# Kernel tuning notes

Hardware: AMD Instinct MI355X
Metric: run time of the kernel (lower is better)

The kernel has to match this reference:

```python
import jax, jax.numpy as jnp
import numpy as np

N, D, C, S = 100000, 512, 4096, 50000


def setup_inputs() -> dict:
    key = jax.random.key(0)
    k1, k2 = jax.random.split(key)
    X = jax.random.normal(k1, (N, D), dtype=jnp.float32)
    codebook_sum = jax.random.normal(k2, (C, D), dtype=jnp.float32)
    prompt_mask = jnp.arange(N) < S  # first S rows are support (True), rest are queries
    return {"X": X, "codebook_sum": codebook_sum, "prompt_mask": prompt_mask, "num_support": S}


def reference(X, codebook_sum, prompt_mask, num_support):
    # num_support is a static Python int (replaces torch.nonzero(prompt_mask) dynamic split)
    s = num_support
    support = X[:s]                                   # [S, D] support (prompt_mask==True)
    query = X[s:]                                     # [Q, D] queries (prompt_mask==False)
    # dense similarity matmul + top-1 nearest-codebook search + gather
    cos_sim = jnp.einsum('sd,cd->sc', support, codebook_sum)  # [S, C]
    top_idx = jnp.argmax(cos_sim, axis=1)             # [S]
    code_n = codebook_sum[top_idx]                    # [S, D] gathered nearest codes
    # mean-pooled prototypes broadcast over queries
    proto = jnp.mean(support, axis=0)                 # [D]
    proto_code = jnp.mean(code_n, axis=0)             # [D]
    # euclidean distances to each prototype
    query_score = jnp.sqrt(jnp.sum((query - proto) ** 2, axis=1))        # [Q]
    query_score_code = jnp.sqrt(jnp.sum((query - proto_code) ** 2, axis=1))  # [Q]
    return (query_score + query_score_code) / 2
```

## Files before the change

### kernel.cpp

```cpp
#include <hip/hip_runtime.h>
#include <hip/hip_bf16.h>

#define NTOT 100000
#define DIM  512
#define CB   4096
#define SSUP 50000
#define NQ   (NTOT - SSUP)

#define MTILES 391
#define MPAD   (MTILES * 128)
#define NTILES 32

typedef __bf16 bf16x8 __attribute__((ext_vector_type(8)));
typedef __bf16 bf16x4 __attribute__((ext_vector_type(4)));
typedef float  f32x4  __attribute__((ext_vector_type(4)));

#define OFF_CBBF   0
#define OFF_XB     4194304
#define OFF_PV     55443456
#define OFF_PI     61849600
#define OFF_PSUM   68255744
#define OFF_PCSUM  68257792
#define OFF_HIST   68259840
#define OFF_TIDX   68276224
#define WS_NEED    (68276224 + 200000)
#define ZERO_BYTES (2048 + 2048 + 16384)

#define F_OFF_PSUM   4194304
#define F_OFF_PCSUM  4196352
#define F_OFF_HIST   4198400
#define F_OFF_TIDX   4214784

__device__ __forceinline__ void load_lds16(const void* g, void* l) {
    __builtin_amdgcn_global_load_lds(
        (const __attribute__((address_space(1))) void*)g,
        (__attribute__((address_space(3))) void*)l, 16, 0, 0);
}

__global__ void k_convert(const float* __restrict__ src, __bf16* __restrict__ dst) {
    int i = (blockIdx.x * 256 + threadIdx.x) * 4;
    float4 v = *(const float4*)(src + i);
    bf16x4 o;
    o[0] = (__bf16)v.x; o[1] = (__bf16)v.y; o[2] = (__bf16)v.z; o[3] = (__bf16)v.w;
    *(bf16x4*)(dst + i) = o;
}

__global__ void k_proto_sum(const float* __restrict__ X, float* __restrict__ protoSum) {
    const int d = threadIdx.x;
    const int r0 = blockIdx.x * 500;
    float acc = 0.f;
    for (int r = r0; r < r0 + 500; ++r)
        acc += X[(size_t)r * DIM + d];
    atomicAdd(&protoSum[d], acc);
}

__global__ __launch_bounds__(256)
void k_gemm_tile(const __bf16* __restrict__ Xb, const __bf16* __restrict__ cbb,
                 float* __restrict__ pv, int* __restrict__ pi)
{
    __shared__ __bf16 lA[128 * 32];
    __shared__ __bf16 lB[128 * 32];
    __shared__ float  sv[128][2];
    __shared__ int    si[128][2];

    const int tid  = threadIdx.x;
    const int wave = tid >> 6;
    const int lane = tid & 63;
    const int wm   = wave >> 1;
    const int wn   = wave & 1;
    const int l15  = lane & 15;
    const int q    = lane >> 4;
    const int nt   = blockIdx.x;
    const int mt   = blockIdx.y;
    const size_t r0 = (size_t)mt * 128;
    const int    c0 = nt * 128;

    f32x4 acc[4][4];
    #pragma unroll
    for (int i = 0; i < 4; ++i)
        #pragma unroll
        for (int j = 0; j < 4; ++j)
            acc[i][j] = (f32x4){0.f, 0.f, 0.f, 0.f};

    for (int k0 = 0; k0 < 512; k0 += 32) {
        __syncthreads();
        #pragma unroll
        for (int i = 0; i < 2; ++i) {
            const int ck  = i * 256 + tid;
            const int row = ck >> 2;
            const int kc  = ck & 3;
            load_lds16(Xb  + (r0 + row) * DIM + k0 + kc * 8, lA + ck * 8);
            load_lds16(cbb + (size_t)(c0 + row) * DIM + k0 + kc * 8, lB + ck * 8);
        }
        __syncthreads();

        bf16x8 af[4], bfr[4];
        #pragma unroll
        for (int t = 0; t < 4; ++t) {
            af[t]  = *(const bf16x8*)(lA + (wm * 64 + t * 16 + l15) * 32 + q * 8);
            bfr[t] = *(const bf16x8*)(lB + (wn * 64 + t * 16 + l15) * 32 + q * 8);
        }
        #pragma unroll
        for (int tm = 0; tm < 4; ++tm)
            #pragma unroll
            for (int tn = 0; tn < 4; ++tn)
                acc[tm][tn] = __builtin_amdgcn_mfma_f32_16x16x32_bf16(
                    af[tm], bfr[tn], acc[tm][tn], 0, 0, 0);
    }

    #pragma unroll
    for (int tm = 0; tm < 4; ++tm) {
        #pragma unroll
        for (int reg = 0; reg < 4; ++reg) {
            float v = -3.0e38f; int idx = 0;
            #pragma unroll
            for (int tn = 0; tn < 4; ++tn) {
                float x = acc[tm][tn][reg];
                int   c = c0 + wn * 64 + tn * 16 + l15;
                if (x > v) { v = x; idx = c; }
            }
            #pragma unroll
            for (int off = 1; off < 16; off <<= 1) {
                float ov = __shfl_xor(v, off, 64);
                int   oi = __shfl_xor(idx, off, 64);
                if (ov > v) { v = ov; idx = oi; }
            }
            if (l15 == 0) {
                int rl = wm * 64 + tm * 16 + q * 4 + reg;
                sv[rl][wn] = v;
                si[rl][wn] = idx;
            }
        }
    }
    __syncthreads();
    if (tid < 128) {
        float v0 = sv[tid][0], v1 = sv[tid][1];
        size_t r = r0 + tid;
        pv[r * 32 + nt] = fmaxf(v0, v1);
        pi[r * 32 + nt] = (v1 > v0) ? si[tid][1] : si[tid][0];
    }
}

__global__ void k_argmax_reduce(const float* __restrict__ pv, const int* __restrict__ pi,
                                int* __restrict__ top_idx) {
    int r = blockIdx.x * 256 + threadIdx.x;
    if (r >= SSUP) return;
    float v = -3.0e38f; int idx = 0;
    #pragma unroll 8
    for (int j = 0; j < 32; ++j) {
        float x = pv[(size_t)r * 32 + j];
        if (x > v) { v = x; idx = pi[(size_t)r * 32 + j]; }
    }
    top_idx[r] = idx;
}

__global__ __launch_bounds__(256, 2)
void k_gemm_argmax(const float* __restrict__ X, const __bf16* __restrict__ cbb,
                   int* __restrict__ top_idx)
{
    __shared__ float redv[64][2];
    __shared__ int   redi[64][2];

    const int tid  = threadIdx.x;
    const int wave = tid >> 6;
    const int lane = tid & 63;
    const int wm   = wave >> 1;
    const int wn   = wave & 1;
    const int l15  = lane & 15;
    const int q    = lane >> 4;
    const int r0   = blockIdx.x * 64;

    bf16x8 aflat[2][16];
    #pragma unroll
    for (int tm = 0; tm < 2; ++tm) {
        const int r = r0 + wm * 32 + tm * 16 + l15;
        const bool valid = (r < SSUP);
        const float* xr = X + (size_t)r * DIM + q * 8;
        #pragma unroll
        for (int kt = 0; kt < 16; ++kt) {
            float4 v0, v1;
            if (valid) {
                v0 = *(const float4*)(xr + kt * 32);
                v1 = *(const float4*)(xr + kt * 32 + 4);
            } else {
                v0 = make_float4(0.f, 0.f, 0.f, 0.f);
                v1 = v0;
            }
            bf16x8 f;
            f[0] = (__bf16)v0.x; f[1] = (__bf16)v0.y; f[2] = (__bf16)v0.z; f[3] = (__bf16)v0.w;
            f[4] = (__bf16)v1.x; f[5] = (__bf16)v1.y; f[6] = (__bf16)v1.z; f[7] = (__bf16)v1.w;
            aflat[tm][kt] = f;
        }
    }

    float mx[8];
    int   mi[8];
    #pragma unroll
    for (int i = 0; i < 8; ++i) { mx[i] = -3.0e38f; mi[i] = 0; }
    const f32x4 zero4 = {0.f, 0.f, 0.f, 0.f};

    for (int ct = 0; ct < 32; ++ct) {
        const int c0 = ct * 128 + wn * 64;
        const __bf16* bptr[4];
        #pragma unroll
        for (int tn = 0; tn < 4; ++tn)
            bptr[tn] = cbb + (size_t)(c0 + tn * 16 + l15) * DIM + q * 8;

        f32x4 acc[2][4];
        #pragma unroll
        for (int i = 0; i < 2; ++i)
            #pragma unroll
            for (int j = 0; j < 4; ++j)
                acc[i][j] = zero4;

        #pragma unroll
        for (int kt = 0; kt < 16; ++kt) {
            bf16x8 b[4];
            #pragma unroll
            for (int tn = 0; tn < 4; ++tn)
                b[tn] = *(const bf16x8*)(bptr[tn] + kt * 32);
            #pragma unroll
            for (int tm = 0; tm < 2; ++tm)
                #pragma unroll
                for (int tn = 0; tn < 4; ++tn)
                    acc[tm][tn] = __builtin_amdgcn_mfma_f32_16x16x32_bf16(
                        aflat[tm][kt], b[tn], acc[tm][tn], 0, 0, 0);
        }
        #pragma unroll
        for (int tm = 0; tm < 2; ++tm)
            #pragma unroll
            for (int tn = 0; tn < 4; ++tn)
                #pragma unroll
                for (int reg = 0; reg < 4; ++reg) {
                    float v = acc[tm][tn][reg];
                    int slot = tm * 4 + reg;
                    int col  = c0 + tn * 16 + l15;
                    if (v > mx[slot]) { mx[slot] = v; mi[slot] = col; }
                }
    }

    #pragma unroll
    for (int slot = 0; slot < 8; ++slot) {
        float v  = mx[slot];
        int  idx = mi[slot];
        #pragma unroll
        for (int off = 1; off < 16; off <<= 1) {
            float ov = __shfl_xor(v, off, 64);
            int   oi = __shfl_xor(idx, off, 64);
            if (ov > v) { v = ov; idx = oi; }
        }
        if (l15 == 0) {
            int rowl = wm * 32 + (slot >> 2) * 16 + q * 4 + (slot & 3);
            redv[rowl][wn] = v;
            redi[rowl][wn] = idx;
        }
    }
    __syncthreads();
    if (tid < 64) {
        int r = r0 + tid;
        if (r < SSUP) {
            float v0 = redv[tid][0], v1 = redv[tid][1];
            top_idx[r] = (v1 > v0) ? redi[tid][1] : redi[tid][0];
        }
    }
}

__global__ void k_hist(const int* __restrict__ top_idx, int* __restrict__ hist) {
    __shared__ int lh[CB];
    for (int i = threadIdx.x; i < CB; i += blockDim.x) lh[i] = 0;
    __syncthreads();
    for (int i = blockIdx.x * blockDim.x + threadIdx.x; i < SSUP; i += gridDim.x * blockDim.x)
        atomicAdd(&lh[top_idx[i]], 1);
    __syncthreads();
    for (int i = threadIdx.x; i < CB; i += blockDim.x) {
        int v = lh[i];
        if (v) atomicAdd(&hist[i], v);
    }
}

__global__ void k_proto_code(const float* __restrict__ cb, const int* __restrict__ hist,
                             float* __restrict__ pcSum) {
    const int d  = threadIdx.x;
    const int c0 = blockIdx.x * 64;
    float acc = 0.f;
    for (int c = c0; c < c0 + 64; ++c) {
        float w = (float)hist[c];
        if (w != 0.f) acc += w * cb[(size_t)c * DIM + d];
    }
    atomicAdd(&pcSum[d], acc);
}

__global__ void k_query(const float* __restrict__ X, const float* __restrict__ protoSum,
                        const float* __restrict__ pcSum, float* __restrict__ out) {
    const int lane   = threadIdx.x & 63;
    const int waveId = (blockIdx.x * blockDim.x + threadIdx.x) >> 6;
    const int nwaves = (gridDim.x * blockDim.x) >> 6;
    const float invS = 1.0f / (float)SSUP;

    for (int r = waveId; r < NQ; r += nwaves) {
        const float* xr = X + (size_t)(SSUP + r) * DIM;
        float s1 = 0.f, s2 = 0.f;
        #pragma unroll
        for (int i = 0; i < 2; ++i) {
            int dd = lane * 4 + i * 256;
            float4 xq = *(const float4*)(xr + dd);
            float4 p  = *(const float4*)(protoSum + dd);
            float4 pc = *(const float4*)(pcSum + dd);
            float d0, d1, d2, d3;
            d0 = xq.x - p.x * invS; d1 = xq.y - p.y * invS;
            d2 = xq.z - p.z * invS; d3 = xq.w - p.w * invS;
            s1 += d0 * d0 + d1 * d1 + d2 * d2 + d3 * d3;
            d0 = xq.x - pc.x * invS; d1 = xq.y - pc.y * invS;
            d2 = xq.z - pc.z * invS; d3 = xq.w - pc.w * invS;
            s2 += d0 * d0 + d1 * d1 + d2 * d2 + d3 * d3;
        }
        #pragma unroll
        for (int off = 32; off > 0; off >>= 1) {
            s1 += __shfl_xor(s1, off, 64);
            s2 += __shfl_xor(s2, off, 64);
        }
        if (lane == 0)
            out[r] = 0.5f * (sqrtf(s1) + sqrtf(s2));
    }
}

extern "C" void kernel_launch(void* const* d_in, const int* in_sizes, int n_in,
                              void* d_out, int out_size, void* d_ws, size_t ws_size,
                              hipStream_t stream) {
    const float* X  = (const float*)d_in[0];
    const float* cb = (const float*)d_in[1];
    float* out = (float*)d_out;
    char* ws = (char*)d_ws;

    __bf16* cbb = (__bf16*)(ws + OFF_CBBF);

    if (ws_size >= (size_t)WS_NEED) {
        __bf16* Xb       = (__bf16*)(ws + OFF_XB);
        float*  pv       = (float*)(ws + OFF_PV);
        int*    pi       = (int*)(ws + OFF_PI);
        float*  protoSum = (float*)(ws + OFF_PSUM);
        float*  pcSum    = (float*)(ws + OFF_PCSUM);
        int*    hist     = (int*)(ws + OFF_HIST);
        int*    top_idx  = (int*)(ws + OFF_TIDX);

        hipMemsetAsync(ws + OFF_PSUM, 0, ZERO_BYTES, stream);

        k_convert<<<(CB * DIM) / 1024, 256, 0, stream>>>(cb, cbb);
        k_convert<<<(MPAD * DIM) / 1024, 256, 0, stream>>>(X, Xb);
        k_proto_sum<<<100, 512, 0, stream>>>(X, protoSum);

        dim3 grid(NTILES, MTILES);
        k_gemm_tile<<<grid, 256, 0, stream>>>(Xb, cbb, pv, pi);

        k_argmax_reduce<<<(SSUP + 255) / 256, 256, 0, stream>>>(pv, pi, top_idx);
        k_hist<<<64, 256, 0, stream>>>(top_idx, hist);
        k_proto_code<<<CB / 64, 512, 0, stream>>>(cb, hist, pcSum);
        k_query<<<1024, 256, 0, stream>>>(X, protoSum, pcSum, out);
    } else {
        float*  protoSum = (float*)(ws + F_OFF_PSUM);
        float*  pcSum    = (float*)(ws + F_OFF_PCSUM);
        int*    hist     = (int*)(ws + F_OFF_HIST);
        int*    top_idx  = (int*)(ws + F_OFF_TIDX);

        hipMemsetAsync(ws + F_OFF_PSUM, 0, ZERO_BYTES, stream);

        k_convert<<<(CB * DIM) / 1024, 256, 0, stream>>>(cb, cbb);
        k_proto_sum<<<100, 512, 0, stream>>>(X, protoSum);
        k_gemm_argmax<<<(SSUP + 63) / 64, 256, 0, stream>>>(X, cbb, top_idx);
        k_hist<<<64, 256, 0, stream>>>(top_idx, hist);
        k_proto_code<<<CB / 64, 512, 0, stream>>>(cb, hist, pcSum);
        k_query<<<1024, 256, 0, stream>>>(X, protoSum, pcSum, out);
    }
}
```

Measured before the change: 621.9 us.

## Double-buffer GEMM with swizzled LDS, fuse convert+protosum and argmax+hist

Replaces the tile GEMM with a double-buffered kernel that uses a K-step of 64, XOR-swizzled LDS layout to avoid bank conflicts, explicit vmcnt waits, MFMA priority boosting, and a swizzled workgroup order for cache locality. It also fuses the X bf16 conversion with the prototype sum, and fuses the per-row argmax reduction with histogram building through an LDS histogram. The aim is to raise MFMA utilization and cut launches and memory passes, at the cost of using 64KB of LDS per block, which may limit occupancy.

```diff
diff --git a/kernel.cpp b/kernel.cpp
--- a/kernel.cpp
+++ b/kernel.cpp
@@ -10,6 +10,8 @@
 #define MTILES 391
 #define MPAD   (MTILES * 128)
 #define NTILES 32
+#define NWG    (MTILES * NTILES)
+#define CPX    (NWG / 8)
 
 typedef __bf16 bf16x8 __attribute__((ext_vector_type(8)));
 typedef __bf16 bf16x4 __attribute__((ext_vector_type(4)));
@@ -37,12 +39,223 @@
         (__attribute__((address_space(3))) void*)l, 16, 0, 0);
 }
 
+#define BARRIER() __builtin_amdgcn_s_barrier()
+#define VMC(N)    asm volatile("s_waitcnt vmcnt(" #N ")" ::: "memory")
+
 __global__ void k_convert(const float* __restrict__ src, __bf16* __restrict__ dst) {
     int i = (blockIdx.x * 256 + threadIdx.x) * 4;
     float4 v = *(const float4*)(src + i);
     bf16x4 o;
     o[0] = (__bf16)v.x; o[1] = (__bf16)v.y; o[2] = (__bf16)v.z; o[3] = (__bf16)v.w;
     *(bf16x4*)(dst + i) = o;
+}
+
+__global__ __launch_bounds__(256)
+void k_conv_psum(const float* __restrict__ X, __bf16* __restrict__ Xb,
+                 float* __restrict__ protoSum)
+{
+    __shared__ float red[4][512];
+    const int tid  = threadIdx.x;
+    const int c8   = (tid & 63) * 8;
+    const int rsub = tid >> 6;
+    const size_t rbase = (size_t)blockIdx.x * 128 + rsub;
+
+    float acc[8];
+    #pragma unroll
+    for (int j = 0; j < 8; ++j) acc[j] = 0.f;
+
+    for (int r = 0; r < 128; r += 4) {
+        const size_t row = rbase + r;
+        const float* p = X + row * DIM + c8;
+        float4 v0 = *(const float4*)p;
+        float4 v1 = *(const float4*)(p + 4);
+        bf16x8 o;
+        o[0] = (__bf16)v0.x; o[1] = (__bf16)v0.y; o[2] = (__bf16)v0.z; o[3] = (__bf16)v0.w;
+        o[4] = (__bf16)v1.x; o[5] = (__bf16)v1.y; o[6] = (__bf16)v1.z; o[7] = (__bf16)v1.w;
+        *(bf16x8*)(Xb + row * DIM + c8) = o;
+        if (row < SSUP) {
+            acc[0] += v0.x; acc[1] += v0.y; acc[2] += v0.z; acc[3] += v0.w;
+            acc[4] += v1.x; acc[5] += v1.y; acc[6] += v1.z; acc[7] += v1.w;
+        }
+    }
+    #pragma unroll
+    for (int j = 0; j < 8; ++j) red[rsub][c8 + j] = acc[j];
+    __syncthreads();
+    if (rsub == 0) {
+        #pragma unroll
+        for (int j = 0; j < 8; ++j)
+            atomicAdd(&protoSum[c8 + j],
+                      red[0][c8 + j] + red[1][c8 + j] + red[2][c8 + j] + red[3][c8 + j]);
+    }
+}
+
+
+template<int MH, int NH>
+__device__ __forceinline__ void mfma_quad_dummy() {}
+
+__global__ __launch_bounds__(256, 2)
+void k_gemm128(const __bf16* __restrict__ Xb, const __bf16* __restrict__ cbb,
+               float* __restrict__ pv, int* __restrict__ pi)
+{
+    __shared__ __align__(16) char lds[65536];
+    __shared__ float sv[128][2];
+    __shared__ int   si[128][2];
+
+    const int tid  = threadIdx.x;
+    const int lane = tid & 63;
+    const int wid  = tid >> 6;
+    const int wm   = wid >> 1;
+    const int wn   = wid & 1;
+    const int l15  = lane & 15;
+    const int q    = lane >> 4;
+
+    const int lin = blockIdx.y * NTILES + blockIdx.x;
+    const int swz = (lin & 7) * CPX + (lin >> 3);
+    const int mt  = swz >> 5;
+    const int nt  = swz & 31;
+    const size_t r0  = (size_t)mt * 128;
+    const size_t c0g = (size_t)nt * 128;
+
+    const int off0 = l15 * 128 + ((q)     ^ (l15 & 7)) * 16;
+    const int off1 = l15 * 128 + ((4 + q) ^ (l15 & 7)) * 16;
+
+    const int ck0 = tid, ck1 = 256 + tid;
+    const int rw0 = ck0 >> 3, rw1 = ck1 >> 3;
+    const int sc0 = (ck0 & 7) ^ (rw0 & 7);
+    const int sc1 = (ck1 & 7) ^ (rw1 & 7);
+    const __bf16* pA0 = Xb  + (r0  + rw0) * DIM + sc0 * 8;
+    const __bf16* pA1 = Xb  + (r0  + rw1) * DIM + sc1 * 8;
+    const __bf16* pB0 = cbb + (c0g + rw0) * DIM + sc0 * 8;
+    const __bf16* pB1 = cbb + (c0g + rw1) * DIM + sc1 * 8;
+    const int d0 = ck0 * 16, d1 = ck1 * 16;
+    const size_t HROW = (size_t)64 * DIM;
+
+    f32x4 acc[4][4];
+    #pragma unroll
+    for (int i = 0; i < 4; ++i)
+        #pragma unroll
+        for (int j = 0; j < 4; ++j)
+            acc[i][j] = (f32x4){0.f, 0.f, 0.f, 0.f};
+
+    auto STAGE = [&](int bufo, int kt) {
+        const int ko = kt * 64;
+        char* lb = lds + bufo;
+        load_lds16(pA0 + ko,        lb + d0);
+        load_lds16(pA1 + ko,        lb + d1);
+        load_lds16(pA0 + HROW + ko, lb + 8192 + d0);
+        load_lds16(pA1 + HROW + ko, lb + 8192 + d1);
+        load_lds16(pB0 + ko,        lb + 16384 + d0);
+        load_lds16(pB1 + ko,        lb + 16384 + d1);
+        load_lds16(pB0 + HROW + ko, lb + 24576 + d0);
+        load_lds16(pB1 + HROW + ko, lb + 24576 + d1);
+    };
+
+    auto COMPUTE = [&](int bufo) {
+        const char* ap = lds + bufo + wm * 8192;
+        const char* bp = lds + bufo + 16384 + wn * 8192;
+        bf16x8 a[4][2], b[4][2];
+        #pragma unroll
+        for (int m = 0; m < 4; ++m) {
+            a[m][0] = *(const bf16x8*)(ap + m * 2048 + off0);
+            a[m][1] = *(const bf16x8*)(ap + m * 2048 + off1);
+        }
+        #pragma unroll
+        for (int n = 0; n < 4; ++n) {
+            b[n][0] = *(const bf16x8*)(bp + n * 2048 + off0);
+            b[n][1] = *(const bf16x8*)(bp + n * 2048 + off1);
+        }
+        __builtin_amdgcn_s_setprio(1);
+        #pragma unroll
+        for (int m = 0; m < 4; ++m)
+            #pragma unroll
+            for (int n = 0; n < 4; ++n)
+                #pragma unroll
+                for (int ks = 0; ks < 2; ++ks)
+                    acc[m][n] = __builtin_amdgcn_mfma_f32_16x16x32_bf16(
+                        a[m][ks], b[n][ks], acc[m][n], 0, 0, 0);
+        __builtin_amdgcn_s_setprio(0);
+    };
+
+    STAGE(0, 0);
+    STAGE(32768, 1);
+    VMC(8);
+    BARRIER();
+
+    #pragma unroll
+    for (int t = 0; t < 6; t += 2) {
+        COMPUTE(0);
+        BARRIER();
+        STAGE(0, t + 2);
+        VMC(8);
+        BARRIER();
+        COMPUTE(32768);
+        BARRIER();
+        STAGE(32768, t + 3);
+        VMC(8);
+        BARRIER();
+    }
+
+    COMPUTE(0);
+    BARRIER();
+    VMC(0);
+    BARRIER();
+    COMPUTE(32768);
+
+    #pragma unroll
+    for (int fm = 0; fm < 4; ++fm) {
+        #pragma unroll
+        for (int reg = 0; reg < 4; ++reg) {
+            float v = -3.0e38f; int idx = 0;
+            #pragma unroll
+            for (int fn = 0; fn < 4; ++fn) {
+                float x = acc[fm][fn][reg];
+                int   c = (int)c0g + wn * 64 + fn * 16 + l15;
+                if (x > v) { v = x; idx = c; }
+            }
+            #pragma unroll
+            for (int off = 1; off < 16; off <<= 1) {
+                float ov = __shfl_xor(v, off, 64);
+                int   oi = __shfl_xor(idx, off, 64);
+                if (ov > v) { v = ov; idx = oi; }
+            }
+            if (l15 == 0) {
+                int rl = wm * 64 + fm * 16 + q * 4 + reg;
+                sv[rl][wn] = v;
+                si[rl][wn] = idx;
+            }
+        }
+    }
+    __syncthreads();
+    if (tid < 128) {
+        float v0 = sv[tid][0], v1 = sv[tid][1];
+        size_t r = r0 + tid;
+        pv[r * 32 + nt] = fmaxf(v0, v1);
+        pi[r * 32 + nt] = (v1 > v0) ? si[tid][1] : si[tid][0];
+    }
+}
+
+__global__ __launch_bounds__(256)
+void k_reduce_hist(const float* __restrict__ pv, const int* __restrict__ pi,
+                   int* __restrict__ hist) {
+    __shared__ int lh[CB];
+    const int tid = threadIdx.x;
+    for (int i = tid; i < CB; i += 256) lh[i] = 0;
+    __syncthreads();
+    const int r = blockIdx.x * 256 + tid;
+    if (r < SSUP) {
+        float v = -3.0e38f; int idx = 0;
+        #pragma unroll 8
+        for (int j = 0; j < 32; ++j) {
+            float x = pv[(size_t)r * 32 + j];
+            if (x > v) { v = x; idx = pi[(size_t)r * 32 + j]; }
+        }
+        atomicAdd(&lh[idx], 1);
+    }
+    __syncthreads();
+    for (int i = tid; i < CB; i += 256) {
+        int v = lh[i];
+        if (v) atomicAdd(&hist[i], v);
+    }
 }
 
 __global__ void k_proto_sum(const float* __restrict__ X, float* __restrict__ protoSum) {
@@ -52,106 +265,6 @@
     for (int r = r0; r < r0 + 500; ++r)
         acc += X[(size_t)r * DIM + d];
     atomicAdd(&protoSum[d], acc);
-}
-
-__global__ __launch_bounds__(256)
-void k_gemm_tile(const __bf16* __restrict__ Xb, const __bf16* __restrict__ cbb,
-                 float* __restrict__ pv, int* __restrict__ pi)
-{
-    __shared__ __bf16 lA[128 * 32];
-    __shared__ __bf16 lB[128 * 32];
-    __shared__ float  sv[128][2];
-    __shared__ int    si[128][2];
-
-    const int tid  = threadIdx.x;
-    const int wave = tid >> 6;
-    const int lane = tid & 63;
-    const int wm   = wave >> 1;
-    const int wn   = wave & 1;
-    const int l15  = lane & 15;
-    const int q    = lane >> 4;
-    const int nt   = blockIdx.x;
-    const int mt   = blockIdx.y;
-    const size_t r0 = (size_t)mt * 128;
-    const int    c0 = nt * 128;
-
-    f32x4 acc[4][4];
-    #pragma unroll
-    for (int i = 0; i < 4; ++i)
-        #pragma unroll
-        for (int j = 0; j < 4; ++j)
-            acc[i][j] = (f32x4){0.f, 0.f, 0.f, 0.f};
-
-    for (int k0 = 0; k0 < 512; k0 += 32) {
-        __syncthreads();
-        #pragma unroll
-        for (int i = 0; i < 2; ++i) {
-            const int ck  = i * 256 + tid;
-            const int row = ck >> 2;
-            const int kc  = ck & 3;
-            load_lds16(Xb  + (r0 + row) * DIM + k0 + kc * 8, lA + ck * 8);
-            load_lds16(cbb + (size_t)(c0 + row) * DIM + k0 + kc * 8, lB + ck * 8);
-        }
-        __syncthreads();
-
-        bf16x8 af[4], bfr[4];
-        #pragma unroll
-        for (int t = 0; t < 4; ++t) {
-            af[t]  = *(const bf16x8*)(lA + (wm * 64 + t * 16 + l15) * 32 + q * 8);
-            bfr[t] = *(const bf16x8*)(lB + (wn * 64 + t * 16 + l15) * 32 + q * 8);
-        }
-        #pragma unroll
-        for (int tm = 0; tm < 4; ++tm)
-            #pragma unroll
-            for (int tn = 0; tn < 4; ++tn)
-                acc[tm][tn] = __builtin_amdgcn_mfma_f32_16x16x32_bf16(
-                    af[tm], bfr[tn], acc[tm][tn], 0, 0, 0);
-    }
-
-    #pragma unroll
-    for (int tm = 0; tm < 4; ++tm) {
-        #pragma unroll
-        for (int reg = 0; reg < 4; ++reg) {
-            float v = -3.0e38f; int idx = 0;
-            #pragma unroll
-            for (int tn = 0; tn < 4; ++tn) {
-                float x = acc[tm][tn][reg];
-                int   c = c0 + wn * 64 + tn * 16 + l15;
-                if (x > v) { v = x; idx = c; }
-            }
-            #pragma unroll
-            for (int off = 1; off < 16; off <<= 1) {
-                float ov = __shfl_xor(v, off, 64);
-                int   oi = __shfl_xor(idx, off, 64);
-                if (ov > v) { v = ov; idx = oi; }
-            }
-            if (l15 == 0) {
-                int rl = wm * 64 + tm * 16 + q * 4 + reg;
-                sv[rl][wn] = v;
-                si[rl][wn] = idx;
-            }
-        }
-    }
-    __syncthreads();
-    if (tid < 128) {
-        float v0 = sv[tid][0], v1 = sv[tid][1];
-        size_t r = r0 + tid;
-        pv[r * 32 + nt] = fmaxf(v0, v1);
-        pi[r * 32 + nt] = (v1 > v0) ? si[tid][1] : si[tid][0];
-    }
-}
-
-__global__ void k_argmax_reduce(const float* __restrict__ pv, const int* __restrict__ pi,
-                                int* __restrict__ top_idx) {
-    int r = blockIdx.x * 256 + threadIdx.x;
-    if (r >= SSUP) return;
-    float v = -3.0e38f; int idx = 0;
-    #pragma unroll 8
-    for (int j = 0; j < 32; ++j) {
-        float x = pv[(size_t)r * 32 + j];
-        if (x > v) { v = x; idx = pi[(size_t)r * 32 + j]; }
-    }
-    top_idx[r] = idx;
 }
 
 __global__ __launch_bounds__(256, 2)
@@ -341,19 +454,16 @@
         float*  protoSum = (float*)(ws + OFF_PSUM);
         float*  pcSum    = (float*)(ws + OFF_PCSUM);
         int*    hist     = (int*)(ws + OFF_HIST);
-        int*    top_idx  = (int*)(ws + OFF_TIDX);
 
         hipMemsetAsync(ws + OFF_PSUM, 0, ZERO_BYTES, stream);
 
         k_convert<<<(CB * DIM) / 1024, 256, 0, stream>>>(cb, cbb);
-        k_convert<<<(MPAD * DIM) / 1024, 256, 0, stream>>>(X, Xb);
-        k_proto_sum<<<100, 512, 0, stream>>>(X, protoSum);
+        k_conv_psum<<<MPAD / 128, 256, 0, stream>>>(X, Xb, protoSum);
 
         dim3 grid(NTILES, MTILES);
-        k_gemm_tile<<<grid, 256, 0, stream>>>(Xb, cbb, pv, pi);
-
-        k_argmax_reduce<<<(SSUP + 255) / 256, 256, 0, stream>>>(pv, pi, top_idx);
-        k_hist<<<64, 256, 0, stream>>>(top_idx, hist);
+        k_gemm128<<<grid, 256, 0, stream>>>(Xb, cbb, pv, pi);
+
+        k_reduce_hist<<<(SSUP + 255) / 256, 256, 0, stream>>>(pv, pi, hist);
         k_proto_code<<<CB / 64, 512, 0, stream>>>(cb, hist, pcSum);
         k_query<<<1024, 256, 0, stream>>>(X, protoSum, pcSum, out);
     } else {
```

After: 681.3 us. 9.6% more time.
